# Kernel optimization log

Measured on AMD Instinct MI355X. Metric: run time of the kernel, lower is better.

Reference implementation:

```python
import jax, jax.numpy as jnp
import numpy as np

B, S, C = 8, 4096, 256
K = 8192  # num_embeddings


def setup_inputs() -> dict:
    key = jax.random.key(0)
    k1, k2 = jax.random.split(key)
    inputs = jax.random.normal(k1, (B, S, C), dtype=jnp.float32)
    # torch init: uniform_(-1/K, 1/K)
    weight = jax.random.uniform(k2, (K, C), dtype=jnp.float32, minval=-1.0 / K, maxval=1.0 / K)
    return {"inputs": inputs, "weight": weight}


def reference(inputs, weight):
    b, s, c = inputs.shape
    flat = inputs.reshape(b * s, c)                       # (N, C)
    distances = (
        jnp.sum(flat * flat, axis=1, keepdims=True)
        + jnp.sum(weight * weight, axis=1)
        - 2.0 * jnp.matmul(flat, weight.T)
    )
    encoding_indices = jnp.argmin(distances, axis=1)      # (N,)
    quantized = weight[encoding_indices].reshape(b, s, c)  # gather == one-hot matmul
    encoding_indices = encoding_indices.reshape(b, s)
    # straight-through estimator
    quantized = inputs + jax.lax.stop_gradient(quantized - inputs)
    return quantized, encoding_indices
```

## Files before the change

### kernel.cpp

```cpp
#include <hip/hip_runtime.h>
#include <hip/hip_fp16.h>

#define N_ROWS 32768
#define KCODES 8192
#define CDIM   256
#define NSUB   (KCODES / 16)
#define MARGIN_DOT 2.2e-4f
#define CAP_BIN 1024
#define SPLIT  4

typedef __attribute__((ext_vector_type(8))) short bf16x8;
typedef __attribute__((ext_vector_type(4))) float f32x4;

#define GLOAD_LDS16(g, l)                                                              \
    __builtin_amdgcn_global_load_lds((const __attribute__((address_space(1))) void*)(g), \
                                     (__attribute__((address_space(3))) void*)(l), 16, 0, 0)

__device__ __forceinline__ ushort f2bf_rne(float f) {
    unsigned u = __float_as_uint(f);
    u += 0x7fffu + ((u >> 16) & 1u);
    return (ushort)(u >> 16);
}

__global__ void prep_kernel(const float* __restrict__ x, const float* __restrict__ wgt,
                            ushort* __restrict__ xb, ushort* __restrict__ wb,
                            float* __restrict__ t1, float* __restrict__ e2,
                            unsigned long long* __restrict__ bestG) {
    const int gtid = blockIdx.x * blockDim.x + threadIdx.x;
    if (gtid < N_ROWS) bestG[gtid] = ~0ull;

    int wave = gtid >> 6;
    int lane = threadIdx.x & 63;
    const float* src; ushort* bdst; float* sqdst; int row;
    if (wave < N_ROWS) { src = x; bdst = xb; sqdst = t1; row = wave; }
    else               { src = wgt; bdst = wb; sqdst = e2; row = wave - N_ROWS; }
    float4 v = *((const float4*)src + (size_t)row * (CDIM / 4) + lane);
    ushort4 o;
    o.x = f2bf_rne(v.x); o.y = f2bf_rne(v.y); o.z = f2bf_rne(v.z); o.w = f2bf_rne(v.w);
    *((ushort4*)bdst + (size_t)row * (CDIM / 4) + lane) = o;
    float s = v.x * v.x + v.y * v.y + v.z * v.z + v.w * v.w;
    for (int off = 32; off; off >>= 1) s += __shfl_down(s, off, 64);
    if (lane == 0) sqdst[row] = s;
}

__launch_bounds__(512, 3)
__global__ void vq_mfma_kernel(const ushort* __restrict__ xb, const ushort* __restrict__ wb,
                               __half* __restrict__ minT) {
    __shared__ ushort xs[2][256 * 32];
    __shared__ ushort ws_l[2][128 * 32];
    ushort (*mbT)[264] = (ushort (*)[264])&xs[0][0];

    const int t = threadIdx.x;
    const int w = t >> 6, lane = t & 63;
    const int ln15 = lane & 15, quad = lane >> 4;
    const int rt = blockIdx.x >> 6;
    const int ct = blockIdx.x & 63;
    const int rbase = (w >> 1) * 64;
    const int cbase = (w & 1) * 64;

    const int srow16 = lane >> 2;
    const int schunk = (lane & 3) ^ ((lane >> 3) & 3);
    const ushort* xsrc = xb + (size_t)(rt * 256 + w * 32 + srow16) * CDIM + schunk * 8;
    const ushort* wsrc = wb + (size_t)(ct * 128 + w * 16 + srow16) * CDIM + schunk * 8;

    f32x4 acc[4][4];
#pragma unroll
    for (int ni = 0; ni < 4; ++ni)
#pragma unroll
        for (int mi = 0; mi < 4; ++mi)
#pragma unroll
            for (int r = 0; r < 4; ++r) acc[ni][mi][r] = 0.f;

#pragma unroll
    for (int j = 0; j < 2; ++j)
        GLOAD_LDS16(xsrc + (size_t)j * 16 * CDIM, &xs[0][(w * 32 + j * 16) * 32]);
    GLOAD_LDS16(wsrc, &ws_l[0][(w * 16) * 32]);
    __syncthreads();

#pragma unroll
    for (int cc = 0; cc < 8; ++cc) {
        const int cur = cc & 1;
        if (cc < 7) {
#pragma unroll
            for (int j = 0; j < 2; ++j)
                GLOAD_LDS16(xsrc + (size_t)j * 16 * CDIM + (cc + 1) * 32,
                            &xs[cur ^ 1][(w * 32 + j * 16) * 32]);
            GLOAD_LDS16(wsrc + (cc + 1) * 32, &ws_l[cur ^ 1][(w * 16) * 32]);
        }
        const int swz = (quad ^ ((ln15 >> 1) & 3)) * 8;
        bf16x8 a[4], b[4];
#pragma unroll
        for (int ni = 0; ni < 4; ++ni)
            a[ni] = *(const bf16x8*)&ws_l[cur][(cbase + ni * 16 + ln15) * 32 + swz];
#pragma unroll
        for (int mi = 0; mi < 4; ++mi)
            b[mi] = *(const bf16x8*)&xs[cur][(rbase + mi * 16 + ln15) * 32 + swz];
#pragma unroll
        for (int ni = 0; ni < 4; ++ni)
#pragma unroll
            for (int mi = 0; mi < 4; ++mi)
                acc[ni][mi] = __builtin_amdgcn_mfma_f32_16x16x32_bf16(a[ni], b[mi], acc[ni][mi], 0, 0, 0);
        __syncthreads();
    }

#pragma unroll
    for (int mi = 0; mi < 4; ++mi) {
        float mxn[4];
#pragma unroll
        for (int ni = 0; ni < 4; ++ni) {
            f32x4 v = acc[ni][mi];
            float mx = fmaxf(fmaxf(v[0], v[1]), fmaxf(v[2], v[3]));
            mx = fmaxf(mx, __shfl_xor(mx, 16, 64));
            mx = fmaxf(mx, __shfl_xor(mx, 32, 64));
            mxn[ni] = mx;
        }
        float sel = quad == 0 ? mxn[0] : quad == 1 ? mxn[1] : quad == 2 ? mxn[2] : mxn[3];
        uint pk = __builtin_bit_cast(uint, __builtin_amdgcn_cvt_pkrtz(sel, sel));
        mbT[(cbase >> 4) + quad][rbase + mi * 16 + ln15] = (ushort)(pk & 0xffffu);
    }
    __syncthreads();
    if (t < 256) {
        union { ushort s[8]; uint4 u; } r;
#pragma unroll
        for (int s = 0; s < 8; ++s) r.s[s] = mbT[s][t];
        *(uint4*)(minT + ((size_t)(rt * 64 + ct) * 256 + t) * 8) = r.u;
    }
}

__launch_bounds__(256, 8)
__global__ void vq_rowmax_kernel(const __half* __restrict__ minT, float* __restrict__ thresh) {
    __shared__ ushort sm[64][136];
    const int t = threadIdx.x, w = t >> 6, lane = t & 63;
    const int row0 = blockIdx.x * 16;

    {
        const int ct = t >> 2, c4 = t & 3;
        const uint4* src = (const uint4*)(minT +
            ((((size_t)(row0 >> 8) * 64 + ct) * 256 + (row0 & 255) + c4 * 4) * 8));
#pragma unroll
        for (int i = 0; i < 4; ++i)
            *(uint4*)&sm[ct][(c4 * 4 + i) * 8] = src[i];
    }
    __syncthreads();

    for (int i = 0; i < 4; ++i) {
        const int rr = w * 4 + i;
        union { uint4 u; __half2 h2[4]; } raw;
        raw.u = *(const uint4*)&sm[lane][rr * 8];
        float m[8];
#pragma unroll
        for (int q = 0; q < 4; ++q) {
            float2 f = __half22float2(raw.h2[q]);
            m[2 * q] = f.x;
            m[2 * q + 1] = f.y;
        }
        float lmax = m[0];
#pragma unroll
        for (int q = 1; q < 8; ++q) lmax = fmaxf(lmax, m[q]);
#pragma unroll
        for (int off = 1; off < 64; off <<= 1) lmax = fmaxf(lmax, __shfl_xor(lmax, off, 64));
        if (lane == 0) thresh[row0 + rr] = lmax - MARGIN_DOT;
    }
}

__launch_bounds__(512, 4)
__global__ void vq_subproc_kernel(const float* __restrict__ x, const float* __restrict__ wgt,
                                  const float* __restrict__ t1, const float* __restrict__ e2,
                                  const __half* __restrict__ minT,
                                  const float* __restrict__ thresh,
                                  unsigned long long* __restrict__ bestG) {
    __shared__ float wsub[16][260];
    __shared__ float xbuf[32][264];
    __shared__ int list[CAP_BIN];
    __shared__ int nlist;

    const int t = threadIdx.x;
    const int g = t >> 4, gl = t & 15;
    const int st = blockIdx.x >> 2;
    const int sp = blockIdx.x & (SPLIT - 1);
    const int ct = st >> 3, sub = st & 7;

    if (t == 0) nlist = 0;
#pragma unroll
    for (int j = 0; j < 2; ++j) {
        const int idx = t + 512 * j;
        *(float4*)&wsub[idx >> 6][(idx & 63) * 4] =
            ((const float4*)(wgt + (size_t)(st * 16 + (idx >> 6)) * CDIM))[idx & 63];
    }
    const float e2v = e2[st * 16 + gl];
    __syncthreads();

    for (int it = 0; it < 16; ++it) {
        const int r = sp * (N_ROWS / SPLIT) + t + 512 * it;
        const uint4 mg = *(const uint4*)(minT +
            ((((size_t)(r >> 8) * 64 + ct) * 256 + (r & 255)) * 8));
        const uint word = (sub >> 1) == 0 ? mg.x : (sub >> 1) == 1 ? mg.y
                        : (sub >> 1) == 2 ? mg.z : mg.w;
        const ushort hbits = (sub & 1) ? (ushort)(word >> 16) : (ushort)(word & 0xffffu);
        const float ms = __half2float(__builtin_bit_cast(__half, hbits));
        if (ms >= thresh[r]) {
            const int pos = atomicAdd(&nlist, 1);
            if (pos < CAP_BIN) {
                list[pos] = r;
            } else {
                const float* xp = x + (size_t)r * CDIM;
                const float t1r = t1[r];
                unsigned long long bk = ~0ull;
                for (int kk = 0; kk < 16; ++kk) {
                    float acc = 0.f;
                    for (int c = 0; c < CDIM; ++c) acc = fmaf(xp[c], wsub[kk][c], acc);
                    float d = (t1r + e2[st * 16 + kk]) - 2.0f * acc;
                    unsigned long long key =
                        ((unsigned long long)__float_as_uint(d) << 32) | (uint)(st * 16 + kk);
                    bk = key < bk ? key : bk;
                }
                atomicMin(&bestG[r], bk);
            }
        }
    }
    __syncthreads();

    const int cnt = nlist < CAP_BIN ? nlist : CAP_BIN;
    for (int base = 0; base < cnt; base += 32) {
        const int e = base + g;
        const bool valid = e < cnt;
        int row = 0;
        if (valid) {
            row = list[e];
            const float4* xs = (const float4*)(x + (size_t)row * CDIM);
#pragma unroll
            for (int j = 0; j < 4; ++j)
                *(float4*)&xbuf[g][(gl + 16 * j) * 4] = xs[gl + 16 * j];
        }
        unsigned long long key = ~0ull;
        if (valid) {
            float acc = 0.f;
#pragma unroll
            for (int c4 = 0; c4 < 64; ++c4) {
                const float4 wv = *(const float4*)&wsub[gl][c4 * 4];
                const float4 xv = *(const float4*)&xbuf[g][c4 * 4];
                acc = fmaf(xv.x, wv.x, acc);
                acc = fmaf(xv.y, wv.y, acc);
                acc = fmaf(xv.z, wv.z, acc);
                acc = fmaf(xv.w, wv.w, acc);
            }
            const int k = st * 16 + gl;
            float d = (t1[row] + e2v) - 2.0f * acc;
            key = ((unsigned long long)__float_as_uint(d) << 32) | (uint)k;
        }
#pragma unroll
        for (int off = 1; off < 16; off <<= 1) {
            unsigned long long ok = __shfl_xor(key, off, 64);
            key = ok < key ? ok : key;
        }
        if (gl == 0 && valid) atomicMin(&bestG[row], key);
    }
}

__launch_bounds__(256, 8)
__global__ void vq_gather_kernel(const float* __restrict__ wgt,
                                 const unsigned long long* __restrict__ bestG,
                                 float* __restrict__ out_q, float* __restrict__ out_i) {
    const int t = threadIdx.x;
    const int g = t >> 4, gl = t & 15;
    const int row = blockIdx.x * 16 + g;
    const int bk = (int)(uint)(bestG[row] & 0xffffffffu);
    if (gl == 0) out_i[row] = (float)bk;
    const float4* src = (const float4*)(wgt + (size_t)bk * CDIM);
    float4* dst = (float4*)(out_q + (size_t)row * CDIM);
#pragma unroll
    for (int j = 0; j < 4; ++j) dst[gl + 16 * j] = src[gl + 16 * j];
}

extern "C" void kernel_launch(void* const* d_in, const int* in_sizes, int n_in,
                              void* d_out, int out_size, void* d_ws, size_t ws_size,
                              hipStream_t stream) {
    const float* x = (const float*)d_in[0];
    const float* wgt = (const float*)d_in[1];

    float* out_q = (float*)d_out;
    float* out_i = out_q + (size_t)N_ROWS * CDIM;

    char* p = (char*)d_ws;
    float* e2 = (float*)p;                     p += (size_t)KCODES * 4;
    float* t1 = (float*)p;                     p += (size_t)N_ROWS * 4;
    __half* minT = (__half*)p;                 p += (size_t)N_ROWS * NSUB * 2;
    ushort* xb = (ushort*)p;                   p += (size_t)N_ROWS * CDIM * 2;
    ushort* wb = (ushort*)p;                   p += (size_t)KCODES * CDIM * 2;
    unsigned long long* bestG = (unsigned long long*)p; p += (size_t)N_ROWS * 8;
    float* thresh = (float*)p;                 p += (size_t)N_ROWS * 4;

    prep_kernel<<<(N_ROWS + KCODES) / 4, 256, 0, stream>>>(x, wgt, xb, wb, t1, e2, bestG);
    vq_mfma_kernel<<<(N_ROWS / 256) * (KCODES / 128), 512, 0, stream>>>(xb, wb, minT);
    vq_rowmax_kernel<<<N_ROWS / 16, 256, 0, stream>>>(minT, thresh);
    vq_subproc_kernel<<<NSUB * SPLIT, 512, 0, stream>>>(x, wgt, t1, e2, minT, thresh, bestG);
    vq_gather_kernel<<<N_ROWS / 16, 256, 0, stream>>>(wgt, bestG, out_q, out_i);
}
```

Measured before the change: 304.0 us.

## Process all eight sub-tiles per block in candidate refinement kernel

Each subproc block now covers a whole 128-code tile (8 sub-tiles of 16) instead of one sub-tile. It reads each minT uint4 once and scatters candidate rows into eight per-sub-tile shared lists. It then loops over sub-tiles, loading each 16-code weight slice into shared memory before refining. This removes the 8x redundant minT and threshold reads and cuts launches from 2048 to 256 blocks. In exchange there is less parallelism (256 blocks on a 256-CU device), lower occupancy from the larger LDS lists, and a slow overflow path that reads weights from global memory.

```diff
diff --git a/kernel.cpp b/kernel.cpp
--- a/kernel.cpp
+++ b/kernel.cpp
@@ -6,7 +6,7 @@
 #define CDIM   256
 #define NSUB   (KCODES / 16)
 #define MARGIN_DOT 2.2e-4f
-#define CAP_BIN 1024
+#define CAP_SUB 768
 #define SPLIT  4
 
 typedef __attribute__((ext_vector_type(8))) short bf16x8;
@@ -163,7 +163,7 @@
     }
 }
 
-__launch_bounds__(512, 4)
+__launch_bounds__(512, 2)
 __global__ void vq_subproc_kernel(const float* __restrict__ x, const float* __restrict__ wgt,
                                   const float* __restrict__ t1, const float* __restrict__ e2,
                                   const __half* __restrict__ minT,
@@ -171,89 +171,103 @@
                                   unsigned long long* __restrict__ bestG) {
     __shared__ float wsub[16][260];
     __shared__ float xbuf[32][264];
-    __shared__ int list[CAP_BIN];
-    __shared__ int nlist;
+    __shared__ int lists[8][CAP_SUB];
+    __shared__ int cnts[8];
 
     const int t = threadIdx.x;
     const int g = t >> 4, gl = t & 15;
-    const int st = blockIdx.x >> 2;
+    const int ct = blockIdx.x >> 2;
     const int sp = blockIdx.x & (SPLIT - 1);
-    const int ct = st >> 3, sub = st & 7;
-
-    if (t == 0) nlist = 0;
-#pragma unroll
-    for (int j = 0; j < 2; ++j) {
-        const int idx = t + 512 * j;
-        *(float4*)&wsub[idx >> 6][(idx & 63) * 4] =
-            ((const float4*)(wgt + (size_t)(st * 16 + (idx >> 6)) * CDIM))[idx & 63];
-    }
-    const float e2v = e2[st * 16 + gl];
+
+    if (t < 8) cnts[t] = 0;
     __syncthreads();
 
     for (int it = 0; it < 16; ++it) {
         const int r = sp * (N_ROWS / SPLIT) + t + 512 * it;
-        const uint4 mg = *(const uint4*)(minT +
-            ((((size_t)(r >> 8) * 64 + ct) * 256 + (r & 255)) * 8));
-        const uint word = (sub >> 1) == 0 ? mg.x : (sub >> 1) == 1 ? mg.y
-                        : (sub >> 1) == 2 ? mg.z : mg.w;
-        const ushort hbits = (sub & 1) ? (ushort)(word >> 16) : (ushort)(word & 0xffffu);
-        const float ms = __half2float(__builtin_bit_cast(__half, hbits));
-        if (ms >= thresh[r]) {
-            const int pos = atomicAdd(&nlist, 1);
-            if (pos < CAP_BIN) {
-                list[pos] = r;
-            } else {
-                const float* xp = x + (size_t)r * CDIM;
-                const float t1r = t1[r];
-                unsigned long long bk = ~0ull;
-                for (int kk = 0; kk < 16; ++kk) {
-                    float acc = 0.f;
-                    for (int c = 0; c < CDIM; ++c) acc = fmaf(xp[c], wsub[kk][c], acc);
-                    float d = (t1r + e2[st * 16 + kk]) - 2.0f * acc;
-                    unsigned long long key =
-                        ((unsigned long long)__float_as_uint(d) << 32) | (uint)(st * 16 + kk);
-                    bk = key < bk ? key : bk;
+        union { uint4 u; __half2 h2[4]; } raw;
+        raw.u = *(const uint4*)(minT + ((((size_t)(r >> 8) * 64 + ct) * 256 + (r & 255)) * 8));
+        const float th = thresh[r];
+        float m[8];
+#pragma unroll
+        for (int q = 0; q < 4; ++q) {
+            float2 f = __half22float2(raw.h2[q]);
+            m[2 * q] = f.x;
+            m[2 * q + 1] = f.y;
+        }
+#pragma unroll
+        for (int s = 0; s < 8; ++s) {
+            if (m[s] >= th) {
+                const int pos = atomicAdd(&cnts[s], 1);
+                if (pos < CAP_SUB) {
+                    lists[s][pos] = r;
+                } else {
+                    const int st = ct * 8 + s;
+                    const float* xp = x + (size_t)r * CDIM;
+                    const float t1r = t1[r];
+                    unsigned long long bk = ~0ull;
+                    for (int kk = 0; kk < 16; ++kk) {
+                        const float* wp = wgt + (size_t)(st * 16 + kk) * CDIM;
+                        float acc = 0.f;
+                        for (int c = 0; c < CDIM; ++c) acc = fmaf(xp[c], wp[c], acc);
+                        float d = (t1r + e2[st * 16 + kk]) - 2.0f * acc;
+                        unsigned long long key =
+                            ((unsigned long long)__float_as_uint(d) << 32) | (uint)(st * 16 + kk);
+                        bk = key < bk ? key : bk;
+                    }
+                    atomicMin(&bestG[r], bk);
                 }
-                atomicMin(&bestG[r], bk);
             }
         }
     }
     __syncthreads();
 
-    const int cnt = nlist < CAP_BIN ? nlist : CAP_BIN;
-    for (int base = 0; base < cnt; base += 32) {
-        const int e = base + g;
-        const bool valid = e < cnt;
-        int row = 0;
-        if (valid) {
-            row = list[e];
-            const float4* xs = (const float4*)(x + (size_t)row * CDIM);
-#pragma unroll
-            for (int j = 0; j < 4; ++j)
-                *(float4*)&xbuf[g][(gl + 16 * j) * 4] = xs[gl + 16 * j];
-        }
-        unsigned long long key = ~0ull;
-        if (valid) {
-            float acc = 0.f;
-#pragma unroll
-            for (int c4 = 0; c4 < 64; ++c4) {
-                const float4 wv = *(const float4*)&wsub[gl][c4 * 4];
-                const float4 xv = *(const float4*)&xbuf[g][c4 * 4];
-                acc = fmaf(xv.x, wv.x, acc);
-                acc = fmaf(xv.y, wv.y, acc);
-                acc = fmaf(xv.z, wv.z, acc);
-                acc = fmaf(xv.w, wv.w, acc);
+    for (int s = 0; s < 8; ++s) {
+        const int st = ct * 8 + s;
+        __syncthreads();
+#pragma unroll
+        for (int j = 0; j < 2; ++j) {
+            const int idx = t + 512 * j;
+            *(float4*)&wsub[idx >> 6][(idx & 63) * 4] =
+                ((const float4*)(wgt + (size_t)(st * 16 + (idx >> 6)) * CDIM))[idx & 63];
+        }
+        __syncthreads();
+        const float e2v = e2[st * 16 + gl];
+        const int cnt = cnts[s] < CAP_SUB ? cnts[s] : CAP_SUB;
+
+        for (int base = 0; base < cnt; base += 32) {
+            const int e = base + g;
+            const bool valid = e < cnt;
+            int row = 0;
+            if (valid) {
+                row = lists[s][e];
+                const float4* xs = (const float4*)(x + (size_t)row * CDIM);
+#pragma unroll
+                for (int j = 0; j < 4; ++j)
+                    *(float4*)&xbuf[g][(gl + 16 * j) * 4] = xs[gl + 16 * j];
             }
-            const int k = st * 16 + gl;
-            float d = (t1[row] + e2v) - 2.0f * acc;
-            key = ((unsigned long long)__float_as_uint(d) << 32) | (uint)k;
-        }
-#pragma unroll
-        for (int off = 1; off < 16; off <<= 1) {
-            unsigned long long ok = __shfl_xor(key, off, 64);
-            key = ok < key ? ok : key;
-        }
-        if (gl == 0 && valid) atomicMin(&bestG[row], key);
+            unsigned long long key = ~0ull;
+            if (valid) {
+                float acc = 0.f;
+#pragma unroll
+                for (int c4 = 0; c4 < 64; ++c4) {
+                    const float4 wv = *(const float4*)&wsub[gl][c4 * 4];
+                    const float4 xv = *(const float4*)&xbuf[g][c4 * 4];
+                    acc = fmaf(xv.x, wv.x, acc);
+                    acc = fmaf(xv.y, wv.y, acc);
+                    acc = fmaf(xv.z, wv.z, acc);
+                    acc = fmaf(xv.w, wv.w, acc);
+                }
+                const int k = st * 16 + gl;
+                float d = (t1[row] + e2v) - 2.0f * acc;
+                key = ((unsigned long long)__float_as_uint(d) << 32) | (uint)k;
+            }
+#pragma unroll
+            for (int off = 1; off < 16; off <<= 1) {
+                unsigned long long ok = __shfl_xor(key, off, 64);
+                key = ok < key ? ok : key;
+            }
+            if (gl == 0 && valid) atomicMin(&bestG[row], key);
+        }
     }
 }
 
@@ -293,6 +307,6 @@
     prep_kernel<<<(N_ROWS + KCODES) / 4, 256, 0, stream>>>(x, wgt, xb, wb, t1, e2, bestG);
     vq_mfma_kernel<<<(N_ROWS / 256) * (KCODES / 128), 512, 0, stream>>>(xb, wb, minT);
     vq_rowmax_kernel<<<N_ROWS / 16, 256, 0, stream>>>(minT, thresh);
-    vq_subproc_kernel<<<NSUB * SPLIT, 512, 0, stream>>>(x, wgt, t1, e2, minT, thresh, bestG);
+    vq_subproc_kernel<<<64 * SPLIT, 512, 0, stream>>>(x, wgt, t1, e2, minT, thresh, bestG);
     vq_gather_kernel<<<N_ROWS / 16, 256, 0, stream>>>(wgt, bestG, out_q, out_i);
 }
```

Measured after the change: 301.3 us. About the same (-0.9%).
